# Kernel optimization log

Hardware: AMD Instinct MI355X
Metric: run time of the kernel (lower is better)

The kernel has to match this reference:

```python
import jax, jax.numpy as jnp
import numpy as np

B_, L_, DM, DS, DC, EX = 4, 2048, 1024, 16, 4, 2
DI = DM * EX

def setup_inputs() -> dict:
    key = jax.random.key(0)
    ks = jax.random.split(key, 8)
    s = lambda i, shape, scale: jax.random.normal(ks[i], shape, jnp.float32) * scale
    return dict(
        x=s(0, (B_, L_, DM), 1.0),
        in_proj_w=s(1, (2 * DI, DM), 0.02),
        conv_weight=s(2, (DI, DC), 0.1),
        conv_bias=jnp.zeros((DI,), jnp.float32),
        A_log=jax.random.uniform(ks[3], (DS,), jnp.float32, -4.0, -1.0),
        D=jnp.ones((DI,), jnp.float32),
        delta_w=s(4, (DS, DI), 0.02),
        delta_b=jnp.ones((DS,), jnp.float32),
        B_w=s(5, (DS, DI), 0.02),
        C_w=s(6, (DS, DI), 0.02),
        out_proj_w=s(7, (DM, DI), 0.02),
    )

def reference(x, in_proj_w, conv_weight, conv_bias, A_log, D, delta_w, delta_b, B_w, C_w, out_proj_w):
    Bb, L, Dm = x.shape
    di, dc = conv_weight.shape
    # 1. input projection and split into ssm / gate branches
    x_inner = x @ in_proj_w.T                       # [B,L,2*di]
    x_ssm, x_gate = x_inner[..., :di], x_inner[..., di:]
    # 2. causal depthwise conv1d + SiLU (kernel size dc, per-channel weights)
    xp = jnp.pad(x_ssm, ((0, 0), (dc - 1, 0), (0, 0)))
    xc = conv_bias + sum(xp[:, k:k + L, :] * conv_weight[:, k] for k in range(dc))
    x_conv = jax.nn.silu(xc)                         # [B,L,di]
    # 3. content-aware discretization
    delta = jax.nn.softplus(x_conv @ delta_w.T + delta_b)  # [B,L,N]
    Bs = x_conv @ B_w.T                              # [B,L,N]
    Cs = x_conv @ C_w.T                              # [B,L,N]
    A = -jnp.exp(A_log)                              # [N]
    xavg = x_conv.mean(axis=-1)                      # [B,L]
    # 4. selective SSM scan over L with state h:[B,N]
    def step(h, inp):
        dt, bt, ct, xa = inp                         # [B,N],[B,N],[B,N],[B]
        h = jnp.exp(dt * A) * h + dt * bt * xa[:, None]
        return h, (h * ct).sum(-1)                   # y_t: [B]
    h0 = jnp.zeros((Bb, A.shape[0]), x.dtype)
    _, ys = jax.lax.scan(
        step, h0,
        (delta.transpose(1, 0, 2), Bs.transpose(1, 0, 2), Cs.transpose(1, 0, 2), xavg.T))
    y_ssm = ys.T[..., None]                          # [B,L,1] (broadcasts over di)
    # 5. gate, skip, output projection
    y_gated = y_ssm * jax.nn.silu(x_gate)
    y_skip = y_gated + x_conv * D
    return y_skip @ out_proj_w.T                     # [B,L,D]
```

## Files before the change

### kernel.cpp

```cpp
#include <hip/hip_runtime.h>
#include <cmath>

#define LL 2048
#define NROW 8192
#define DMODEL 1024
#define DINNER 2048
#define NSTATE 16
#define NSEG 64
#define SEGLEN 32

typedef unsigned short u16;
typedef __attribute__((ext_vector_type(8))) unsigned short u16x8;
typedef __attribute__((ext_vector_type(8))) short short8;
typedef __attribute__((ext_vector_type(4))) float floatx4;
typedef __attribute__((ext_vector_type(16))) float floatx16;

__device__ __forceinline__ float bf2f(u16 h) {
    unsigned u = ((unsigned)h) << 16;
    float f;
    __builtin_memcpy(&f, &u, 4);
    return f;
}
__device__ __forceinline__ u16 f2bf(float f) {
    unsigned u;
    __builtin_memcpy(&u, &f, 4);
    u = u + 0x7fffu + ((u >> 16) & 1u);
    return (u16)(u >> 16);
}
__device__ __forceinline__ float silu_f(float x) { return x / (1.f + __expf(-x)); }

__global__ __launch_bounds__(256) void cvt_multi(
    const float* __restrict__ s0, const float* __restrict__ s1,
    const float* __restrict__ s2, const float* __restrict__ s3,
    const float* __restrict__ s4, const float* __restrict__ s5,
    u16* __restrict__ d0, u16* __restrict__ d1, u16* __restrict__ d2,
    u16* __restrict__ d3, u16* __restrict__ d4, u16* __restrict__ d5) {
    int bid = blockIdx.x;
    const float* s;
    u16* d;
    size_t off;
    if (bid < 4096)      { s = s0; d = d0; off = (size_t)bid * 2048; }
    else if (bid < 6144) { s = s1; d = d1; off = (size_t)(bid - 4096) * 2048; }
    else if (bid < 7168) { s = s2; d = d2; off = (size_t)(bid - 6144) * 2048; }
    else if (bid < 7184) { s = s3; d = d3; off = (size_t)(bid - 7168) * 2048; }
    else if (bid < 7200) { s = s4; d = d4; off = (size_t)(bid - 7184) * 2048; }
    else                 { s = s5; d = d5; off = (size_t)(bid - 7200) * 2048; }
    size_t i = off + (size_t)threadIdx.x * 8;
    float4 a = *(const float4*)&s[i];
    float4 b = *(const float4*)&s[i + 4];
    u16x8 o;
    o[0] = f2bf(a.x); o[1] = f2bf(a.y); o[2] = f2bf(a.z); o[3] = f2bf(a.w);
    o[4] = f2bf(b.x); o[5] = f2bf(b.y); o[6] = f2bf(b.z); o[7] = f2bf(b.w);
    *(u16x8*)&d[i] = o;
}

#define GL_LDS(gp, lp)                                                        \
    __builtin_amdgcn_global_load_lds(                                         \
        (const __attribute__((address_space(1))) void*)(gp),                  \
        (__attribute__((address_space(3))) void*)(lp), 16, 0, 0)
#define BAR() __builtin_amdgcn_s_barrier()
#define SB0() __builtin_amdgcn_sched_barrier(0)
#define LGKM0()                                                               \
    do {                                                                      \
        asm volatile("s_waitcnt lgkmcnt(0)" ::: "memory");                    \
        __builtin_amdgcn_sched_barrier(0);                                    \
    } while (0)
#define VMC4() asm volatile("s_waitcnt vmcnt(4)" ::: "memory")
#define PRIO1() __builtin_amdgcn_s_setprio(1)
#define PRIO0() __builtin_amdgcn_s_setprio(0)

template <int OUT_BF16>
__global__ __launch_bounds__(512, 2) void gemm_bt_256(
    const u16* __restrict__ A, const u16* __restrict__ B,
    void* __restrict__ Cout, int N, int K) {
    __shared__ u16 sAf[2 * 2 * 128 * 64];
    __shared__ u16 sBf[2 * 2 * 128 * 64];
    const int tid = threadIdx.x;
    const int lane = tid & 63;
    const int wave = tid >> 6;
    const int wm = wave >> 2;
    const int wn = wave & 3;

    const int gx = gridDim.x;
    const int nwg = gx * gridDim.y;
    const int cpx = nwg >> 3;
    int lin = blockIdx.y * gx + blockIdx.x;
    int swz = (lin & 7) * cpx + (lin >> 3);
    const int bm = (swz / gx) * 256;
    const int bn = (swz % gx) * 256;

    const int gslot = (lane & 7) ^ ((lane >> 3) & 7);
    const int srowoff = lane >> 3;
    const u16* aStage = A + (size_t)(bm + wave * 8 + srowoff) * K + gslot * 8 + 64;
    const u16* bStage = B + (size_t)(bn + wave * 8 + srowoff) * K + gslot * 8 + 128;
    const size_t row64 = (size_t)64 * K;
    const size_t row128 = (size_t)128 * K;

#define STAGE_A(BUF, H, PTR)                                                  \
    do {                                                                      \
        GL_LDS((PTR) + (H) * row128,         &sAf[(BUF) * 16384 + (H) * 8192 + wave * 512]); \
        GL_LDS((PTR) + (H) * row128 + row64, &sAf[(BUF) * 16384 + (H) * 8192 + (8 + wave) * 512]); \
    } while (0)
#define STAGE_B(BUF, H, PTR)                                                  \
    do {                                                                      \
        GL_LDS((PTR) + (H) * row128,         &sBf[(BUF) * 16384 + (H) * 8192 + wave * 512]); \
        GL_LDS((PTR) + (H) * row128 + row64, &sBf[(BUF) * 16384 + (H) * 8192 + (8 + wave) * 512]); \
    } while (0)

    const int fr = lane & 15;
    const int kq = lane >> 4;
    const int st0 = kq ^ (fr & 7);
    const int st1 = (4 + kq) ^ (fr & 7);
    const int aRd0 = wm * 8192 + fr * 64 + st0 * 8;
    const int aRd1 = wm * 8192 + fr * 64 + st1 * 8;
    const int bRow = (wn & 1) * 64 + fr;
    const int bRd0 = (wn >> 1) * 8192 + bRow * 64 + st0 * 8;
    const int bRd1 = (wn >> 1) * 8192 + bRow * 64 + st1 * 8;

#define RD_A(dst, BUF, R0)                                                    \
    do {                                                                      \
        _Pragma("unroll")                                                     \
        for (int mi = 0; mi < 4; ++mi) {                                      \
            dst[mi][0] = *(const short8*)&sAf[(BUF) * 16384 + aRd0 + ((R0) + mi * 16) * 64]; \
            dst[mi][1] = *(const short8*)&sAf[(BUF) * 16384 + aRd1 + ((R0) + mi * 16) * 64]; \
        }                                                                     \
    } while (0)
#define RD_B(dst, BUF, R0)                                                    \
    do {                                                                      \
        _Pragma("unroll")                                                     \
        for (int ni = 0; ni < 2; ++ni) {                                      \
            dst[ni][0] = *(const short8*)&sBf[(BUF) * 16384 + bRd0 + ((R0) + ni * 16) * 64]; \
            dst[ni][1] = *(const short8*)&sBf[(BUF) * 16384 + bRd1 + ((R0) + ni * 16) * 64]; \
        }                                                                     \
    } while (0)
#define MFMA_PH(AF, RB, BF, CB)                                               \
    do {                                                                      \
        _Pragma("unroll")                                                     \
        for (int kh = 0; kh < 2; ++kh)                                        \
            _Pragma("unroll")                                                 \
            for (int mi = 0; mi < 4; ++mi)                                    \
                _Pragma("unroll")                                             \
                for (int ni = 0; ni < 2; ++ni)                                \
                    acc[(RB) + mi][(CB) + ni] =                               \
                        __builtin_amdgcn_mfma_f32_16x16x32_bf16(              \
                            AF[mi][kh], BF[ni][kh],                           \
                            acc[(RB) + mi][(CB) + ni], 0, 0, 0);              \
    } while (0)

    floatx4 acc[8][4];
#pragma unroll
    for (int i = 0; i < 8; ++i)
#pragma unroll
        for (int j = 0; j < 4; ++j) acc[i][j] = (floatx4){0.f, 0.f, 0.f, 0.f};

    short8 afX[4][2], afY[4][2], bf01[2][2], bf23[2][2];

    {
        const u16* a0 = aStage - 64;
        const u16* b0 = bStage - 128;
        STAGE_A(0, 0, a0);
        STAGE_A(0, 1, a0);
        STAGE_B(0, 0, b0);
        STAGE_B(0, 1, b0);
        STAGE_B(1, 0, b0 + 64);
        STAGE_B(1, 1, b0 + 64);
    }
    VMC4();
    BAR();
    RD_A(afX, 0, 0);
    RD_B(bf01, 0, 0);
    SB0();

#define TILE(CUR, NXT)                                                        \
                  \
    LGKM0();                                                                  \
    PRIO1();                                                                  \
    MFMA_PH(afX, 0, bf01, 0);                                                 \
    PRIO0();                                                                  \
    SB0();                                                                    \
    RD_B(bf23, CUR, 32);                                                      \
    STAGE_A(NXT, 0, aStage);                                                  \
    SB0();                                                                    \
         \
    LGKM0();                                                                  \
    PRIO1();                                                                  \
    MFMA_PH(afX, 0, bf23, 2);                                                 \
    PRIO0();                                                                  \
    SB0();                                                                    \
    RD_A(afY, CUR, 64);                                                       \
    STAGE_A(NXT, 1, aStage);                                                  \
    VMC4();                                                \
    BAR();                                                                    \
                 \
    LGKM0();                                                                  \
    PRIO1();                                                                  \
    MFMA_PH(afY, 4, bf01, 0);                                                 \
    PRIO0();                                                                  \
    SB0();                                                                    \
    RD_B(bf01, NXT, 0);                                                       \
    STAGE_B(CUR, 0, bStage);                                                  \
    SB0();                                                                    \
             \
    PRIO1();                                                                  \
    MFMA_PH(afY, 4, bf23, 2);                                                 \
    PRIO0();                                                                  \
    SB0();                                                                    \
    STAGE_B(CUR, 1, bStage);                                                  \
    VMC4();                                                \
    BAR();                                                                    \
    RD_A(afX, NXT, 0);                                                        \
    SB0();                                                                    \
    aStage += 64;                                                             \
    bStage += 64;

    const int NT = K >> 6;
    for (int t = 0; t < NT; t += 2) {
        TILE(0, 1)
        TILE(1, 0)
    }
#undef TILE

    const int cc = lane & 15;
    const int rb = (lane >> 4) * 4;
#pragma unroll
    for (int mi = 0; mi < 8; ++mi)
#pragma unroll
        for (int ni = 0; ni < 4; ++ni)
#pragma unroll
            for (int r = 0; r < 4; ++r) {
                int grow = bm + wm * 128 + mi * 16 + rb + r;
                int gcol = bn + wn * 64 + ni * 16 + cc;
                float v = acc[mi][ni][r];
                if (OUT_BF16)
                    ((u16*)Cout)[(size_t)grow * N + gcol] = f2bf(v);
                else
                    ((float*)Cout)[(size_t)grow * N + gcol] = v;
            }
#undef STAGE_A
#undef STAGE_B
#undef RD_A
#undef RD_B
#undef MFMA_PH
}

template <int OUT_BF16>
__global__ __launch_bounds__(256) void gemm_bt_mfma(
    const u16* __restrict__ A, const u16* __restrict__ B,
    void* __restrict__ Cout, int N, int K) {
    __shared__ u16 As[128 * 32];
    __shared__ u16 Bs[128 * 32];
    const int tid = threadIdx.x;
    const int lane = tid & 63;
    const int wave = tid >> 6;
    const int bm = blockIdx.y * 128;
    const int bn = blockIdx.x * 128;

    const int kbg = (lane & 3) ^ ((lane >> 3) & 3);
    const int srow = lane >> 2;
    const u16* ag[2];
    const u16* bg[2];
#pragma unroll
    for (int p = 0; p < 2; ++p) {
        int c = wave * 2 + p;
        ag[p] = A + (size_t)(bm + c * 16 + srow) * K + kbg * 8;
        bg[p] = B + (size_t)(bn + c * 16 + srow) * K + kbg * 8;
    }
    const int frow = lane & 31;
    const int khi = lane >> 5;
    const int wr = (wave >> 1) * 64;
    const int wc = (wave & 1) * 64;
    int aoff[2][2], boff[2][2];
#pragma unroll
    for (int mi = 0; mi < 2; ++mi)
#pragma unroll
        for (int kh = 0; kh < 2; ++kh) {
            int rA = wr + mi * 32 + frow;
            int rB = wc + mi * 32 + frow;
            int kb = kh * 2 + khi;
            aoff[mi][kh] = rA * 32 + (kb ^ ((rA >> 1) & 3)) * 8;
            boff[mi][kh] = rB * 32 + (kb ^ ((rB >> 1) & 3)) * 8;
        }
    floatx16 acc[2][2];
#pragma unroll
    for (int i = 0; i < 2; ++i)
#pragma unroll
        for (int j = 0; j < 2; ++j) acc[i][j] = (floatx16)(0.f);

    for (int k0 = 0; k0 < K; k0 += 32) {
        __syncthreads();
#pragma unroll
        for (int p = 0; p < 2; ++p) {
            int c = wave * 2 + p;
            __builtin_amdgcn_global_load_lds(
                (const __attribute__((address_space(1))) void*)ag[p],
                (__attribute__((address_space(3))) void*)&As[c * 512], 16, 0, 0);
            __builtin_amdgcn_global_load_lds(
                (const __attribute__((address_space(1))) void*)bg[p],
                (__attribute__((address_space(3))) void*)&Bs[c * 512], 16, 0, 0);
            ag[p] += 32;
            bg[p] += 32;
        }
        __syncthreads();
        short8 af[2][2], bf[2][2];
#pragma unroll
        for (int mi = 0; mi < 2; ++mi)
#pragma unroll
            for (int kh = 0; kh < 2; ++kh) {
                af[mi][kh] = *(const short8*)&As[aoff[mi][kh]];
                bf[mi][kh] = *(const short8*)&Bs[boff[mi][kh]];
            }
#pragma unroll
        for (int kh = 0; kh < 2; ++kh)
#pragma unroll
            for (int mi = 0; mi < 2; ++mi)
#pragma unroll
                for (int ni = 0; ni < 2; ++ni)
                    acc[mi][ni] = __builtin_amdgcn_mfma_f32_32x32x16_bf16(
                        af[mi][kh], bf[ni][kh], acc[mi][ni], 0, 0, 0);
    }
    const int cc = lane & 31;
    const int rbase = 4 * (lane >> 5);
#pragma unroll
    for (int mi = 0; mi < 2; ++mi)
#pragma unroll
        for (int ni = 0; ni < 2; ++ni)
#pragma unroll
            for (int r = 0; r < 16; ++r) {
                int grow = bm + wr + mi * 32 + (r & 3) + 8 * (r >> 2) + rbase;
                int gcol = bn + wc + ni * 32 + cc;
                float v = acc[mi][ni][r];
                if (OUT_BF16)
                    ((u16*)Cout)[(size_t)grow * N + gcol] = f2bf(v);
                else
                    ((float*)Cout)[(size_t)grow * N + gcol] = v;
            }
}

__global__ __launch_bounds__(256) void conv_silu_avg(
    const u16* __restrict__ xin, const float* __restrict__ cw,
    const float* __restrict__ cb, u16* __restrict__ xconv,
    float* __restrict__ xavg) {
    const int blk = blockIdx.x;
    const int b = blk >> 7;
    const int lc = blk & 127;
    const int row0 = b * LL + lc * 16;
    const int tid = threadIdx.x;
    const int lane = tid & 63, wave = tid >> 6;
    const int d0 = tid * 8;
    float4 cwv[8];
    float cbv[8];
#pragma unroll
    for (int e = 0; e < 8; ++e) cwv[e] = *(const float4*)&cw[(d0 + e) * 4];
#pragma unroll
    for (int e = 0; e < 8; e += 4) {
        float4 c = *(const float4*)&cb[d0 + e];
        cbv[e] = c.x; cbv[e + 1] = c.y; cbv[e + 2] = c.z; cbv[e + 3] = c.w;
    }
    u16x8 w0, w1, w2;
    if (lc == 0) {
        w0 = (u16x8)0; w1 = (u16x8)0; w2 = (u16x8)0;
    } else {
        w0 = *(const u16x8*)&xin[(size_t)(row0 - 3) * (2 * DINNER) + d0];
        w1 = *(const u16x8*)&xin[(size_t)(row0 - 2) * (2 * DINNER) + d0];
        w2 = *(const u16x8*)&xin[(size_t)(row0 - 1) * (2 * DINNER) + d0];
    }
    float sums[16];
#pragma unroll
    for (int t = 0; t < 16; ++t) {
        u16x8 cur = *(const u16x8*)&xin[(size_t)(row0 + t) * (2 * DINNER) + d0];
        float lsum = 0.f;
        u16x8 o;
#pragma unroll
        for (int e = 0; e < 8; ++e) {
            float acc = cbv[e];
            acc += bf2f(w0[e]) * cwv[e].x;
            acc += bf2f(w1[e]) * cwv[e].y;
            acc += bf2f(w2[e]) * cwv[e].z;
            acc += bf2f(cur[e]) * cwv[e].w;
            float s = silu_f(acc);
            lsum += s;
            o[e] = f2bf(s);
        }
        *(u16x8*)&xconv[(size_t)(row0 + t) * DINNER + d0] = o;
        sums[t] = lsum;
        w0 = w1; w1 = w2; w2 = cur;
    }
#pragma unroll
    for (int off = 32; off; off >>= 1)
#pragma unroll
        for (int t = 0; t < 16; ++t) sums[t] += __shfl_down(sums[t], off);
    __shared__ float wred[4][16];
    if (lane == 0) {
#pragma unroll
        for (int t = 0; t < 16; ++t) wred[wave][t] = sums[t];
    }
    __syncthreads();
    if (tid < 16)
        xavg[row0 + tid] = (wred[0][tid] + wred[1][tid] + wred[2][tid] + wred[3][tid]) *
                           (1.f / DINNER);
}

__global__ __launch_bounds__(256) void dbc_direct(
    const u16* __restrict__ xconv, const u16* __restrict__ wcat,
    const float* __restrict__ db, const float* __restrict__ A_log,
    const float* __restrict__ xavg,
    float* __restrict__ a_out, float* __restrict__ u_out, float* __restrict__ c_out) {
    __shared__ float part[4][32][48];
    const int tid = threadIdx.x;
    const int lane = tid & 63;
    const int wave = tid >> 6;
    const int bm = blockIdx.x * 32;
    const int fr = lane & 15;
    const int kq = lane >> 4;
    const int k0 = wave * 512 + kq * 8;

    const u16* ap0 = xconv + (size_t)(bm + fr) * DINNER + k0;
    const u16* ap1 = xconv + (size_t)(bm + 16 + fr) * DINNER + k0;
    const u16* bp0 = wcat + (size_t)(fr) * DINNER + k0;
    const u16* bp1 = wcat + (size_t)(16 + fr) * DINNER + k0;
    const u16* bp2 = wcat + (size_t)(32 + fr) * DINNER + k0;

    floatx4 acc[2][3];
#pragma unroll
    for (int mi = 0; mi < 2; ++mi)
#pragma unroll
        for (int ni = 0; ni < 3; ++ni) acc[mi][ni] = (floatx4){0.f, 0.f, 0.f, 0.f};

#pragma unroll 4
    for (int kk = 0; kk < 16; ++kk) {
        short8 a0 = *(const short8*)ap0;
        short8 a1 = *(const short8*)ap1;
        short8 b0 = *(const short8*)bp0;
        short8 b1 = *(const short8*)bp1;
        short8 b2 = *(const short8*)bp2;
        ap0 += 32; ap1 += 32; bp0 += 32; bp1 += 32; bp2 += 32;
        acc[0][0] = __builtin_amdgcn_mfma_f32_16x16x32_bf16(a0, b0, acc[0][0], 0, 0, 0);
        acc[0][1] = __builtin_amdgcn_mfma_f32_16x16x32_bf16(a0, b1, acc[0][1], 0, 0, 0);
        acc[0][2] = __builtin_amdgcn_mfma_f32_16x16x32_bf16(a0, b2, acc[0][2], 0, 0, 0);
        acc[1][0] = __builtin_amdgcn_mfma_f32_16x16x32_bf16(a1, b0, acc[1][0], 0, 0, 0);
        acc[1][1] = __builtin_amdgcn_mfma_f32_16x16x32_bf16(a1, b1, acc[1][1], 0, 0, 0);
        acc[1][2] = __builtin_amdgcn_mfma_f32_16x16x32_bf16(a1, b2, acc[1][2], 0, 0, 0);
    }
    const int cr = kq * 4;
#pragma unroll
    for (int mi = 0; mi < 2; ++mi)
#pragma unroll
        for (int ni = 0; ni < 3; ++ni)
#pragma unroll
            for (int r = 0; r < 4; ++r)
                part[wave][mi * 16 + cr + r][ni * 16 + fr] = acc[mi][ni][r];
    __syncthreads();
#pragma unroll
    for (int it = tid; it < 512; it += 256) {
        int row = it >> 4;
        int s = it & 15;
        float sd = 0.f, sb = 0.f, sc = 0.f;
#pragma unroll
        for (int w = 0; w < 4; ++w) {
            sd += part[w][row][s];
            sb += part[w][row][s + 16];
            sc += part[w][row][s + 32];
        }
        int grow = bm + row;
        float Aa = -__expf(A_log[s]);
        float pre = sd + db[s];
        float delta = (pre > 20.f) ? pre : log1pf(__expf(pre));
        a_out[grow * NSTATE + s] = __expf(delta * Aa);
        u_out[grow * NSTATE + s] = delta * sb * xavg[grow];
        c_out[grow * NSTATE + s] = sc;
    }
}

__global__ __launch_bounds__(1024) void scan_fused(
    const float* __restrict__ a, const float* __restrict__ u,
    const float* __restrict__ c, float* __restrict__ y) {
    const int b = blockIdx.x;
    const int tid = threadIdx.x;
    const int s = tid & 15;
    const int seg = tid >> 4;
    __shared__ float Ps[NSEG][NSTATE];
    __shared__ float Hs[NSEG][NSTATE];
    __shared__ float HSs[NSEG][NSTATE];

    size_t base = (size_t)(b * LL + seg * SEGLEN) * NSTATE + s;
    float P = 1.f, h = 0.f;
#pragma unroll 8
    for (int t = 0; t < SEGLEN; ++t) {
        float av = a[base + (size_t)t * NSTATE];
        float uv = u[base + (size_t)t * NSTATE];
        h = fmaf(av, h, uv);
        P *= av;
    }
    Ps[seg][s] = P;
    Hs[seg][s] = h;
    __syncthreads();
    if (tid < 16) {
        float hh = 0.f;
        for (int g = 0; g < NSEG; ++g) {
            HSs[g][tid] = hh;
            hh = fmaf(Ps[g][tid], hh, Hs[g][tid]);
        }
    }
    __syncthreads();
    float h2 = HSs[seg][s];
#pragma unroll 8
    for (int t = 0; t < SEGLEN; ++t) {
        float av = a[base + (size_t)t * NSTATE];
        float uv = u[base + (size_t)t * NSTATE];
        float cv = c[base + (size_t)t * NSTATE];
        h2 = fmaf(av, h2, uv);
        float p = h2 * cv;
        p += __shfl_xor(p, 1);
        p += __shfl_xor(p, 2);
        p += __shfl_xor(p, 4);
        p += __shfl_xor(p, 8);
        if (s == 0) y[b * LL + seg * SEGLEN + t] = p;
    }
}

__global__ __launch_bounds__(256) void gate_skip(
    const u16* __restrict__ xin, const float* __restrict__ y,
    const float* __restrict__ Dv, const u16* __restrict__ xconv,
    u16* __restrict__ yskip) {
    size_t i = ((size_t)blockIdx.x * 256 + threadIdx.x) * 8;
    int row = (int)(i >> 11);
    int d = (int)(i & (DINNER - 1));
    u16x8 g = *(const u16x8*)&xin[(size_t)row * (2 * DINNER) + DINNER + d];
    u16x8 xc = *(const u16x8*)&xconv[i];
    float yv = y[row];
    u16x8 o;
#pragma unroll
    for (int e = 0; e < 8; ++e) {
        float gv = silu_f(bf2f(g[e]));
        float v = yv * gv + bf2f(xc[e]) * Dv[d + e];
        o[e] = f2bf(v);
    }
    *(u16x8*)&yskip[i] = o;
}

extern "C" void kernel_launch(void* const* d_in, const int* in_sizes, int n_in,
                              void* d_out, int out_size, void* d_ws, size_t ws_size,
                              hipStream_t stream) {
    const float* x       = (const float*)d_in[0];
    const float* w_in    = (const float*)d_in[1];
    const float* conv_w  = (const float*)d_in[2];
    const float* conv_b  = (const float*)d_in[3];
    const float* A_log   = (const float*)d_in[4];
    const float* Dv      = (const float*)d_in[5];
    const float* delta_w = (const float*)d_in[6];
    const float* delta_b = (const float*)d_in[7];
    const float* B_w     = (const float*)d_in[8];
    const float* C_w     = (const float*)d_in[9];
    const float* out_w   = (const float*)d_in[10];
    float* out = (float*)d_out;

    u16* xb  = (u16*)d_ws;
    u16* wb  = xb + 8388608;
    u16* owb = wb + 4194304;
    u16* wsb = owb + 2097152;
    u16* xin = wsb + 98304;
    u16* xcv = xin + 33554432;
    u16* ysk = xcv + 16777216;
    float* fb     = (float*)(ysk + 16777216);
    float* abuf   = fb;
    float* ubuf   = abuf + 131072;
    float* cbuf   = ubuf + 131072;
    float* ybuf   = cbuf + 131072;
    float* avgbuf = ybuf + 8192;

    cvt_multi<<<7216, 256, 0, stream>>>(x, w_in, out_w, delta_w, B_w, C_w,
                                        xb, wb, owb, wsb, wsb + 32768, wsb + 65536);

    gemm_bt_256<1><<<dim3(16, 32), 512, 0, stream>>>(xb, wb, xin, 2 * DINNER, DMODEL);

    conv_silu_avg<<<512, 256, 0, stream>>>(xin, conv_w, conv_b, xcv, avgbuf);
    dbc_direct<<<256, 256, 0, stream>>>(xcv, wsb, delta_b, A_log, avgbuf,
                                        abuf, ubuf, cbuf);

    scan_fused<<<4, 1024, 0, stream>>>(abuf, ubuf, cbuf, ybuf);

    gate_skip<<<NROW * DINNER / 8 / 256, 256, 0, stream>>>(xin, ybuf, Dv, xcv, ysk);

    gemm_bt_mfma<0><<<dim3(8, 64), 256, 0, stream>>>(ysk, owb, out, DMODEL, DINNER);
}
```

Baseline: 302.1 us.

## Switch big GEMM to 32x32x16 MFMA and remap blocks across XCDs

The main 256-wide GEMM kernel now uses 32x32x16 bf16 MFMA tiles instead of 16x16x32. It changes the LDS fragment read pattern, the accumulator layout and the epilogue indexing to match. Larger MFMA tiles cut the number of LDS fragment reads per flop and the instruction count. Separately, the smaller gemm_bt_mfma kernel remaps block indices so consecutive tiles are spread across the 8 XCDs, which should improve L2 locality. Both changes risk bank conflicts under the new swizzle and shift register pressure.

```diff
diff --git a/kernel.cpp b/kernel.cpp
--- a/kernel.cpp
+++ b/kernel.cpp
@@ -107,53 +107,47 @@
         GL_LDS((PTR) + (H) * row128 + row64, &sBf[(BUF) * 16384 + (H) * 8192 + (8 + wave) * 512]); \
     } while (0)
 
-    const int fr = lane & 15;
-    const int kq = lane >> 4;
-    const int st0 = kq ^ (fr & 7);
-    const int st1 = (4 + kq) ^ (fr & 7);
-    const int aRd0 = wm * 8192 + fr * 64 + st0 * 8;
-    const int aRd1 = wm * 8192 + fr * 64 + st1 * 8;
-    const int bRow = (wn & 1) * 64 + fr;
-    const int bRd0 = (wn >> 1) * 8192 + bRow * 64 + st0 * 8;
-    const int bRd1 = (wn >> 1) * 8192 + bRow * 64 + st1 * 8;
-
-#define RD_A(dst, BUF, R0)                                                    \
+    const int fcol = lane & 31;
+    const int khalf = lane >> 5;
+    int aS[4];
+#pragma unroll
+    for (int ks = 0; ks < 4; ++ks) aS[ks] = ((ks * 2 + khalf) ^ (fcol & 7)) * 8;
+    const int aRow = wm * 8192 + fcol * 64;
+    const int bRow = (wn >> 1) * 8192 + ((wn & 1) * 64 + fcol) * 64;
+
+#define RD_A2(dst, BUF, R0)                                                   \
     do {                                                                      \
         _Pragma("unroll")                                                     \
-        for (int mi = 0; mi < 4; ++mi) {                                      \
-            dst[mi][0] = *(const short8*)&sAf[(BUF) * 16384 + aRd0 + ((R0) + mi * 16) * 64]; \
-            dst[mi][1] = *(const short8*)&sAf[(BUF) * 16384 + aRd1 + ((R0) + mi * 16) * 64]; \
-        }                                                                     \
+        for (int m = 0; m < 2; ++m)                                           \
+            _Pragma("unroll")                                                 \
+            for (int ks = 0; ks < 4; ++ks)                                    \
+                dst[m][ks] = *(const short8*)&sAf[(BUF) * 16384 + aRow +      \
+                                                  ((R0) + m * 32) * 64 + aS[ks]]; \
     } while (0)
-#define RD_B(dst, BUF, R0)                                                    \
+#define RD_B1(dst, BUF, NI)                                                   \
     do {                                                                      \
         _Pragma("unroll")                                                     \
-        for (int ni = 0; ni < 2; ++ni) {                                      \
-            dst[ni][0] = *(const short8*)&sBf[(BUF) * 16384 + bRd0 + ((R0) + ni * 16) * 64]; \
-            dst[ni][1] = *(const short8*)&sBf[(BUF) * 16384 + bRd1 + ((R0) + ni * 16) * 64]; \
-        }                                                                     \
+        for (int ks = 0; ks < 4; ++ks)                                        \
+            dst[ks] = *(const short8*)&sBf[(BUF) * 16384 + bRow +             \
+                                           (NI) * 32 * 64 + aS[ks]];          \
     } while (0)
-#define MFMA_PH(AF, RB, BF, CB)                                               \
+#define MFMA8(AF, MB, BF, NI)                                                 \
     do {                                                                      \
         _Pragma("unroll")                                                     \
-        for (int kh = 0; kh < 2; ++kh)                                        \
+        for (int ks = 0; ks < 4; ++ks)                                        \
             _Pragma("unroll")                                                 \
-            for (int mi = 0; mi < 4; ++mi)                                    \
-                _Pragma("unroll")                                             \
-                for (int ni = 0; ni < 2; ++ni)                                \
-                    acc[(RB) + mi][(CB) + ni] =                               \
-                        __builtin_amdgcn_mfma_f32_16x16x32_bf16(              \
-                            AF[mi][kh], BF[ni][kh],                           \
-                            acc[(RB) + mi][(CB) + ni], 0, 0, 0);              \
+            for (int m = 0; m < 2; ++m)                                       \
+                acc[(MB) + m][NI] = __builtin_amdgcn_mfma_f32_32x32x16_bf16(  \
+                    AF[m][ks], BF[ks], acc[(MB) + m][NI], 0, 0, 0);           \
     } while (0)
 
-    floatx4 acc[8][4];
-#pragma unroll
-    for (int i = 0; i < 8; ++i)
-#pragma unroll
-        for (int j = 0; j < 4; ++j) acc[i][j] = (floatx4){0.f, 0.f, 0.f, 0.f};
-
-    short8 afX[4][2], afY[4][2], bf01[2][2], bf23[2][2];
+    floatx16 acc[4][2];
+#pragma unroll
+    for (int i = 0; i < 4; ++i)
+#pragma unroll
+        for (int j = 0; j < 2; ++j) acc[i][j] = (floatx16)(0.f);
+
+    short8 afX[2][4], afY[2][4], bf0[4], bf1[4];
 
     {
         const u16* a0 = aStage - 64;
@@ -167,48 +161,48 @@
     }
     VMC4();
     BAR();
-    RD_A(afX, 0, 0);
-    RD_B(bf01, 0, 0);
+    RD_A2(afX, 0, 0);
+    RD_B1(bf0, 0, 0);
     SB0();
 
 #define TILE(CUR, NXT)                                                        \
-                  \
+                     \
     LGKM0();                                                                  \
     PRIO1();                                                                  \
-    MFMA_PH(afX, 0, bf01, 0);                                                 \
+    MFMA8(afX, 0, bf0, 0);                                                    \
     PRIO0();                                                                  \
     SB0();                                                                    \
-    RD_B(bf23, CUR, 32);                                                      \
+    RD_B1(bf1, CUR, 1);                                                       \
     STAGE_A(NXT, 0, aStage);                                                  \
     SB0();                                                                    \
-         \
+           \
     LGKM0();                                                                  \
     PRIO1();                                                                  \
-    MFMA_PH(afX, 0, bf23, 2);                                                 \
+    MFMA8(afX, 0, bf1, 1);                                                    \
     PRIO0();                                                                  \
     SB0();                                                                    \
-    RD_A(afY, CUR, 64);                                                       \
+    RD_A2(afY, CUR, 64);                                                      \
     STAGE_A(NXT, 1, aStage);                                                  \
     VMC4();                                                \
     BAR();                                                                    \
-                 \
+                    \
     LGKM0();                                                                  \
     PRIO1();                                                                  \
-    MFMA_PH(afY, 4, bf01, 0);                                                 \
+    MFMA8(afY, 2, bf0, 0);                                                    \
     PRIO0();                                                                  \
     SB0();                                                                    \
-    RD_B(bf01, NXT, 0);                                                       \
+    RD_B1(bf0, NXT, 0);                                                       \
     STAGE_B(CUR, 0, bStage);                                                  \
     SB0();                                                                    \
-             \
+          \
     PRIO1();                                                                  \
-    MFMA_PH(afY, 4, bf23, 2);                                                 \
+    MFMA8(afY, 2, bf1, 1);                                                    \
     PRIO0();                                                                  \
     SB0();                                                                    \
     STAGE_B(CUR, 1, bStage);                                                  \
     VMC4();                                                \
     BAR();                                                                    \
-    RD_A(afX, NXT, 0);                                                        \
+    RD_A2(afX, NXT, 0);                                                       \
     SB0();                                                                    \
     aStage += 64;                                                             \
     bStage += 64;
@@ -220,16 +214,15 @@
     }
 #undef TILE
 
-    const int cc = lane & 15;
-    const int rb = (lane >> 4) * 4;
-#pragma unroll
-    for (int mi = 0; mi < 8; ++mi)
-#pragma unroll
-        for (int ni = 0; ni < 4; ++ni)
-#pragma unroll
-            for (int r = 0; r < 4; ++r) {
-                int grow = bm + wm * 128 + mi * 16 + rb + r;
-                int gcol = bn + wn * 64 + ni * 16 + cc;
+    const int erow = 4 * khalf;
+#pragma unroll
+    for (int mi = 0; mi < 4; ++mi)
+#pragma unroll
+        for (int ni = 0; ni < 2; ++ni)
+#pragma unroll
+            for (int r = 0; r < 16; ++r) {
+                int grow = bm + wm * 128 + mi * 32 + (r & 3) + 8 * (r >> 2) + erow;
+                int gcol = bn + wn * 64 + ni * 32 + fcol;
                 float v = acc[mi][ni][r];
                 if (OUT_BF16)
                     ((u16*)Cout)[(size_t)grow * N + gcol] = f2bf(v);
@@ -238,9 +231,9 @@
             }
 #undef STAGE_A
 #undef STAGE_B
-#undef RD_A
-#undef RD_B
-#undef MFMA_PH
+#undef RD_A2
+#undef RD_B1
+#undef MFMA8
 }
 
 template <int OUT_BF16>
@@ -252,8 +245,16 @@
     const int tid = threadIdx.x;
     const int lane = tid & 63;
     const int wave = tid >> 6;
-    const int bm = blockIdx.y * 128;
-    const int bn = blockIdx.x * 128;
+
+    const int gx = gridDim.x;
+    const int nwg = gx * gridDim.y;
+    int lin = blockIdx.y * gx + blockIdx.x;
+    if ((nwg & 7) == 0) {
+        int cpx = nwg >> 3;
+        lin = (lin & 7) * cpx + (lin >> 3);
+    }
+    const int bm = (lin / gx) * 128;
+    const int bn = (lin % gx) * 128;
 
     const int kbg = (lane & 3) ^ ((lane >> 3) & 3);
     const int srow = lane >> 2;
```

Measured after the change: 304.6 us. About the same (+0.8%).

## Replace out-projection GEMM with double-buffered 512-thread pipelined 128x128 kernel

Applied to the files above, without the earlier changes.

The output projection GEMM moves from a simple single-buffered 256-thread 32x32 MFMA kernel that synchronises twice per K step to a 512-thread, 64-wide K tile kernel. The new kernel double-buffers LDS, uses 16x16x32 MFMAs with XOR-swizzled LDS reads and an L2-friendly workgroup swizzle, and interleaves async global-to-LDS staging with MFMA phases. The aim is to hide global load latency and raise MFMA utilisation. The cost is more complex barrier and waitcnt ordering and more LDS per block.

```diff
diff --git a/kernel.cpp b/kernel.cpp
--- a/kernel.cpp
+++ b/kernel.cpp
@@ -66,6 +66,7 @@
         __builtin_amdgcn_sched_barrier(0);                                    \
     } while (0)
 #define VMC4() asm volatile("s_waitcnt vmcnt(4)" ::: "memory")
+#define VMC2() asm volatile("s_waitcnt vmcnt(2)" ::: "memory")
 #define PRIO1() __builtin_amdgcn_s_setprio(1)
 #define PRIO0() __builtin_amdgcn_s_setprio(0)
 
@@ -172,7 +173,7 @@
     SB0();
 
 #define TILE(CUR, NXT)                                                        \
-                  \
+                      \
     LGKM0();                                                                  \
     PRIO1();                                                                  \
     MFMA_PH(afX, 0, bf01, 0);                                                 \
@@ -181,7 +182,7 @@
     RD_B(bf23, CUR, 32);                                                      \
     STAGE_A(NXT, 0, aStage);                                                  \
     SB0();                                                                    \
-         \
+             \
     LGKM0();                                                                  \
     PRIO1();                                                                  \
     MFMA_PH(afX, 0, bf23, 2);                                                 \
@@ -191,7 +192,7 @@
     STAGE_A(NXT, 1, aStage);                                                  \
     VMC4();                                                \
     BAR();                                                                    \
-                 \
+                     \
     LGKM0();                                                                  \
     PRIO1();                                                                  \
     MFMA_PH(afY, 4, bf01, 0);                                                 \
@@ -200,7 +201,7 @@
     RD_B(bf01, NXT, 0);                                                       \
     STAGE_B(CUR, 0, bStage);                                                  \
     SB0();                                                                    \
-             \
+            \
     PRIO1();                                                                  \
     MFMA_PH(afY, 4, bf23, 2);                                                 \
     PRIO0();                                                                  \
@@ -244,96 +245,146 @@
 }
 
 template <int OUT_BF16>
-__global__ __launch_bounds__(256) void gemm_bt_mfma(
+__global__ __launch_bounds__(512, 4) void gemm_bt_128p(
     const u16* __restrict__ A, const u16* __restrict__ B,
     void* __restrict__ Cout, int N, int K) {
-    __shared__ u16 As[128 * 32];
-    __shared__ u16 Bs[128 * 32];
+    __shared__ u16 sAf[2 * 128 * 64];
+    __shared__ u16 sBf[2 * 128 * 64];
     const int tid = threadIdx.x;
     const int lane = tid & 63;
     const int wave = tid >> 6;
-    const int bm = blockIdx.y * 128;
-    const int bn = blockIdx.x * 128;
-
-    const int kbg = (lane & 3) ^ ((lane >> 3) & 3);
-    const int srow = lane >> 2;
-    const u16* ag[2];
-    const u16* bg[2];
-#pragma unroll
-    for (int p = 0; p < 2; ++p) {
-        int c = wave * 2 + p;
-        ag[p] = A + (size_t)(bm + c * 16 + srow) * K + kbg * 8;
-        bg[p] = B + (size_t)(bn + c * 16 + srow) * K + kbg * 8;
-    }
-    const int frow = lane & 31;
-    const int khi = lane >> 5;
-    const int wr = (wave >> 1) * 64;
-    const int wc = (wave & 1) * 64;
-    int aoff[2][2], boff[2][2];
-#pragma unroll
-    for (int mi = 0; mi < 2; ++mi)
-#pragma unroll
-        for (int kh = 0; kh < 2; ++kh) {
-            int rA = wr + mi * 32 + frow;
-            int rB = wc + mi * 32 + frow;
-            int kb = kh * 2 + khi;
-            aoff[mi][kh] = rA * 32 + (kb ^ ((rA >> 1) & 3)) * 8;
-            boff[mi][kh] = rB * 32 + (kb ^ ((rB >> 1) & 3)) * 8;
-        }
-    floatx16 acc[2][2];
-#pragma unroll
-    for (int i = 0; i < 2; ++i)
-#pragma unroll
-        for (int j = 0; j < 2; ++j) acc[i][j] = (floatx16)(0.f);
-
-    for (int k0 = 0; k0 < K; k0 += 32) {
-        __syncthreads();
-#pragma unroll
-        for (int p = 0; p < 2; ++p) {
-            int c = wave * 2 + p;
-            __builtin_amdgcn_global_load_lds(
-                (const __attribute__((address_space(1))) void*)ag[p],
-                (__attribute__((address_space(3))) void*)&As[c * 512], 16, 0, 0);
-            __builtin_amdgcn_global_load_lds(
-                (const __attribute__((address_space(1))) void*)bg[p],
-                (__attribute__((address_space(3))) void*)&Bs[c * 512], 16, 0, 0);
-            ag[p] += 32;
-            bg[p] += 32;
-        }
-        __syncthreads();
-        short8 af[2][2], bf[2][2];
-#pragma unroll
-        for (int mi = 0; mi < 2; ++mi)
-#pragma unroll
-            for (int kh = 0; kh < 2; ++kh) {
-                af[mi][kh] = *(const short8*)&As[aoff[mi][kh]];
-                bf[mi][kh] = *(const short8*)&Bs[boff[mi][kh]];
-            }
-#pragma unroll
-        for (int kh = 0; kh < 2; ++kh)
-#pragma unroll
-            for (int mi = 0; mi < 2; ++mi)
-#pragma unroll
-                for (int ni = 0; ni < 2; ++ni)
-                    acc[mi][ni] = __builtin_amdgcn_mfma_f32_32x32x16_bf16(
-                        af[mi][kh], bf[ni][kh], acc[mi][ni], 0, 0, 0);
-    }
-    const int cc = lane & 31;
-    const int rbase = 4 * (lane >> 5);
-#pragma unroll
-    for (int mi = 0; mi < 2; ++mi)
+    const int wm = wave >> 2;
+    const int wn = wave & 3;
+
+    const int gx = gridDim.x;
+    const int nwg = gx * gridDim.y;
+    const int cpx = nwg >> 3;
+    int lin = blockIdx.y * gx + blockIdx.x;
+    int swz = (lin & 7) * cpx + (lin >> 3);
+    const int bm = (swz / gx) * 128;
+    const int bn = (swz % gx) * 128;
+
+    const int gslot = (lane & 7) ^ ((lane >> 3) & 7);
+    const int srowoff = lane >> 3;
+    const u16* aStage = A + (size_t)(bm + wave * 8 + srowoff) * K + gslot * 8 + 64;
+    const u16* bStage = B + (size_t)(bn + wave * 8 + srowoff) * K + gslot * 8 + 128;
+    const size_t row64 = (size_t)64 * K;
+
+#define STAGE_A(BUF, PTR)                                                     \
+    do {                                                                      \
+        GL_LDS((PTR),         &sAf[(BUF) * 8192 + wave * 512]);               \
+        GL_LDS((PTR) + row64, &sAf[(BUF) * 8192 + (8 + wave) * 512]);         \
+    } while (0)
+#define STAGE_B(BUF, PTR)                                                     \
+    do {                                                                      \
+        GL_LDS((PTR),         &sBf[(BUF) * 8192 + wave * 512]);               \
+        GL_LDS((PTR) + row64, &sBf[(BUF) * 8192 + (8 + wave) * 512]);         \
+    } while (0)
+
+    const int fr = lane & 15;
+    const int kq = lane >> 4;
+    const int st0 = kq ^ (fr & 7);
+    const int st1 = (4 + kq) ^ (fr & 7);
+    const int aRd0 = (wm * 64 + fr) * 64 + st0 * 8;
+    const int aRd1 = (wm * 64 + fr) * 64 + st1 * 8;
+    const int bRd0 = (wn * 32 + fr) * 64 + st0 * 8;
+    const int bRd1 = (wn * 32 + fr) * 64 + st1 * 8;
+
+#define RD_A(dst, BUF)                                                        \
+    do {                                                                      \
+        _Pragma("unroll")                                                     \
+        for (int mi = 0; mi < 4; ++mi) {                                      \
+            dst[mi][0] = *(const short8*)&sAf[(BUF) * 8192 + aRd0 + mi * 16 * 64]; \
+            dst[mi][1] = *(const short8*)&sAf[(BUF) * 8192 + aRd1 + mi * 16 * 64]; \
+        }                                                                     \
+    } while (0)
+#define RD_B(dst, BUF, NI)                                                    \
+    do {                                                                      \
+        dst[0] = *(const short8*)&sBf[(BUF) * 8192 + bRd0 + (NI) * 16 * 64];  \
+        dst[1] = *(const short8*)&sBf[(BUF) * 8192 + bRd1 + (NI) * 16 * 64];  \
+    } while (0)
+#define MFMA8(BF, NI)                                                         \
+    do {                                                                      \
+        _Pragma("unroll")                                                     \
+        for (int kh = 0; kh < 2; ++kh)                                        \
+            _Pragma("unroll")                                                 \
+            for (int mi = 0; mi < 4; ++mi)                                    \
+                acc[mi][NI] = __builtin_amdgcn_mfma_f32_16x16x32_bf16(        \
+                    afc[mi][kh], BF[kh], acc[mi][NI], 0, 0, 0);               \
+    } while (0)
+
+    floatx4 acc[4][2];
+#pragma unroll
+    for (int i = 0; i < 4; ++i)
+#pragma unroll
+        for (int j = 0; j < 2; ++j) acc[i][j] = (floatx4){0.f, 0.f, 0.f, 0.f};
+
+    short8 afc[4][2], bf0[2], bf1[2];
+
+    STAGE_A(0, aStage - 64);
+    STAGE_B(0, bStage - 128);
+    STAGE_B(1, bStage - 64);
+    VMC2();
+    BAR();
+    RD_A(afc, 0);
+    RD_B(bf0, 0, 0);
+    SB0();
+
+#define TILE(CUR, NXT)                                                        \
+                              \
+    LGKM0();                                                                  \
+    PRIO1();                                                                  \
+    MFMA8(bf0, 0);                                                            \
+    PRIO0();                                                                  \
+    SB0();                                                                    \
+    RD_B(bf1, CUR, 1);                                                        \
+    STAGE_A(NXT, aStage);                                                     \
+    BAR();                                                                    \
+                  \
+    LGKM0();                                                                  \
+    PRIO1();                                                                  \
+    MFMA8(bf1, 1);                                                            \
+    PRIO0();                                                                  \
+    SB0();                                                                    \
+    STAGE_B(CUR, bStage);                                                     \
+    VMC2();                      \
+    BAR();                                                                    \
+    RD_A(afc, NXT);                                                           \
+    RD_B(bf0, NXT, 0);                                                        \
+    SB0();                                                                    \
+    aStage += 64;                                                             \
+    bStage += 64;
+
+    const int NT = K >> 6;
+    for (int t = 0; t < NT; t += 2) {
+        TILE(0, 1)
+        TILE(1, 0)
+    }
+#undef TILE
+
+    asm volatile("s_waitcnt vmcnt(0)" ::: "memory");
+
+    const int cc = lane & 15;
+    const int rb = (lane >> 4) * 4;
+#pragma unroll
+    for (int mi = 0; mi < 4; ++mi)
 #pragma unroll
         for (int ni = 0; ni < 2; ++ni)
 #pragma unroll
-            for (int r = 0; r < 16; ++r) {
-                int grow = bm + wr + mi * 32 + (r & 3) + 8 * (r >> 2) + rbase;
-                int gcol = bn + wc + ni * 32 + cc;
+            for (int r = 0; r < 4; ++r) {
+                int grow = bm + wm * 64 + mi * 16 + rb + r;
+                int gcol = bn + wn * 32 + ni * 16 + cc;
                 float v = acc[mi][ni][r];
                 if (OUT_BF16)
                     ((u16*)Cout)[(size_t)grow * N + gcol] = f2bf(v);
                 else
                     ((float*)Cout)[(size_t)grow * N + gcol] = v;
             }
+#undef STAGE_A
+#undef STAGE_B
+#undef RD_A
+#undef RD_B
+#undef MFMA8
 }
 
 __global__ __launch_bounds__(256) void conv_silu_avg(
@@ -581,5 +632,5 @@
 
     gate_skip<<<NROW * DINNER / 8 / 256, 256, 0, stream>>>(xin, ybuf, Dv, xcv, ysk);
 
-    gemm_bt_mfma<0><<<dim3(8, 64), 256, 0, stream>>>(ysk, owb, out, DMODEL, DINNER);
-}
+    gemm_bt_128p<0><<<dim3(8, 64), 512, 0, stream>>>(ysk, owb, out, DMODEL, DINNER);
+}
```

Measured after the change: 288.5 us. -4.5%, faster.
